# Optimization experiments

Hardware: AMD Instinct MI355X
Metric: run time of the kernel (lower is better)

## Reference

```python
import jax, jax.numpy as jnp
import numpy as np

NUM_HEADS = 12
NUM_LANDMARKS = 64
PINV_ITERS = 6


def moore_penrose_iter_pinv(x, iters=PINV_ITERS):
    # x: [..., m, m]
    abs_x = jnp.abs(x)
    col = abs_x.sum(axis=-1)
    row = abs_x.sum(axis=-2)
    z = jnp.swapaxes(x, -1, -2) / (jnp.max(col) * jnp.max(row))
    I = jnp.eye(x.shape[-1], dtype=x.dtype)
    for _ in range(iters):
        xz = x @ z
        z = 0.25 * z @ (13.0 * I - xz @ (15.0 * I - xz @ (7.0 * I - xz)))
    return z


def setup_inputs() -> dict:
    key = jax.random.key(0)
    k1, k2, k3, k4 = jax.random.split(key, 4)
    B, N, C = 2, 2048, 768
    x = jax.random.normal(k1, (B, N, C), dtype=jnp.float32)
    w_qkv = jax.random.normal(k2, (3 * C, C), dtype=jnp.float32) * 0.02
    w_proj = jax.random.normal(k3, (C, C), dtype=jnp.float32) * 0.02
    b_proj = jax.random.normal(k4, (C,), dtype=jnp.float32) * 0.02
    return {"x": x, "w_qkv": w_qkv, "w_proj": w_proj, "b_proj": b_proj}


def reference(x, w_qkv, w_proj, b_proj):
    B, N, C = x.shape
    H = NUM_HEADS
    m = NUM_LANDMARKS
    d = C // H
    scale = d ** -0.5
    original_N = N

    rem = N % m
    if rem > 0:  # pad at the FRONT of the sequence, as in the torch code
        x = jnp.pad(x, ((0, 0), (m - rem, 0), (0, 0)))
        N = x.shape[1]

    qkv = x @ w_qkv.T  # [B, N, 3C]
    q, k, v = jnp.split(qkv, 3, axis=-1)
    # [B, N, C] -> [B, H, N, d]
    to_heads = lambda t: t.reshape(B, N, H, d).transpose(0, 2, 1, 3)
    q, k, v = to_heads(q), to_heads(k), to_heads(v)
    q = q * scale

    l = N // m  # segment length per landmark (N is a multiple of m after padding)
    # '(n l) d -> n d' mean over l: landmarks [B, H, m, d]
    q_landmarks = q.reshape(B, H, m, l, d).mean(axis=3)
    k_landmarks = k.reshape(B, H, m, l, d).mean(axis=3)

    sim1 = jnp.einsum('bhnd,bhmd->bhnm', q, k_landmarks)          # [B,H,N,m]
    sim2 = jnp.einsum('bhid,bhjd->bhij', q_landmarks, k_landmarks)  # [B,H,m,m]
    sim3 = jnp.einsum('bhmd,bhnd->bhmn', q_landmarks, k)          # [B,H,m,N]

    attn1 = jax.nn.softmax(sim1, axis=-1)
    attn2 = jax.nn.softmax(sim2, axis=-1)
    attn3 = jax.nn.softmax(sim3, axis=-1)

    attn2_inv = moore_penrose_iter_pinv(attn2, PINV_ITERS)

    attn = (attn1 @ attn2_inv) @ attn3            # [B,H,N,N] full attention map
    out = attn1 @ (attn2_inv @ (attn3 @ v))       # [B,H,N,d]

    out = out.transpose(0, 2, 1, 3).reshape(B, N, C)
    out = out[:, -original_N:]
    out = out @ w_proj.T + b_proj
    return out, attn
```

## Files before the change

### kernel.cpp

```cpp
#include <hip/hip_runtime.h>
#include <math.h>

#define BQ 2
#define NQ 2048
#define CQ 768
#define HQ 12
#define DQ 64
#define MQ 64
#define LQ 32
#define C3 2304
#define BH 24
#define BN 4096

typedef short bf16x8 __attribute__((ext_vector_type(8)));
typedef float f32x4 __attribute__((ext_vector_type(4)));

__device__ inline void atomicMaxPosF(float* addr, float v) {
  atomicMax((int*)addr, __float_as_int(v));
}

__device__ inline void f2pair(float f, ushort& hi, ushort& lo) {
  union { float f; unsigned u; } a; a.f = f;
  hi = (ushort)(a.u >> 16);
  union { unsigned u; float f; } h; h.u = ((unsigned)hi) << 16;
  union { float f; unsigned u; } b; b.f = f - h.f;
  lo = (ushort)(b.u >> 16);
}

__device__ inline void stage_plane(const ushort* __restrict__ g, int ld,
                                   ushort* l, int t) {
#pragma unroll
  for (int i = 0; i < 4; ++i) {
    int flat = t + i * 256;
    int row = flat >> 3;
    int ch = (flat & 7) ^ (row & 7);
    __builtin_amdgcn_global_load_lds(
        (const __attribute__((address_space(1))) void*)(g + (size_t)row * ld + ch * 8),
        (__attribute__((address_space(3))) void*)(l + flat * 8), 16, 0, 0);
  }
}

__device__ inline bf16x8 rdfrag(const ushort* p, int row, int kb) {
  return *(const bf16x8*)((const char*)p + row * 128 + (kb ^ ((row & 7) << 4)));
}

__global__ __launch_bounds__(256) void gemm_bt3(
    const ushort* __restrict__ Ah, const ushort* __restrict__ Al,
    const ushort* __restrict__ Bh, const ushort* __restrict__ Bl,
    const float* __restrict__ bias, float* __restrict__ C,
    int Kdim, int lda, int ldb, int ldc, int qscale, int zH,
    long long sAb, long long sAh, long long sBb, long long sBh,
    long long sCb, long long sCh)
{
  __shared__ __align__(16) ushort lds[32768];
  ushort* LAh = lds;
  ushort* LAl = lds + 8192;
  ushort* LBh = lds + 16384;
  ushort* LBl = lds + 24576;
  const int t = threadIdx.x;
  const int z = blockIdx.z;
  const int b = z / zH, h = z % zH;
  const size_t aoff = (size_t)b * sAb + (size_t)h * sAh + (size_t)blockIdx.x * 128 * lda;
  const size_t boff = (size_t)b * sBb + (size_t)h * sBh + (size_t)blockIdx.y * 128 * ldb;
  const ushort* pAh = Ah + aoff;
  const ushort* pAl = Al + aoff;
  const ushort* pBh = Bh + boff;
  const ushort* pBl = Bl + boff;
  float* Cp = C + (size_t)b * sCb + (size_t)h * sCh;
  const int lane = t & 63, wv = t >> 6, wm = wv >> 1, wn = wv & 1;
  f32x4 zz = {0.f, 0.f, 0.f, 0.f};
  f32x4 acc[4][4] = {{zz, zz, zz, zz}, {zz, zz, zz, zz},
                     {zz, zz, zz, zz}, {zz, zz, zz, zz}};
  for (int k0 = 0; k0 < Kdim; k0 += 64) {
    stage_plane(pAh + k0, lda, LAh, t);
    stage_plane(pAl + k0, lda, LAl, t);
    stage_plane(pBh + k0, ldb, LBh, t);
    stage_plane(pBl + k0, ldb, LBl, t);
    __syncthreads();
#pragma unroll
    for (int kh = 0; kh < 2; ++kh) {
      const int kb = kh * 64 + ((lane >> 4) * 16);
      bf16x8 aH[4], aL[4], bHf[4], bLf[4];
#pragma unroll
      for (int i = 0; i < 4; ++i) {
        int ra = wm * 64 + i * 16 + (lane & 15);
        int rb = wn * 64 + i * 16 + (lane & 15);
        aH[i] = rdfrag(LAh, ra, kb);
        aL[i] = rdfrag(LAl, ra, kb);
        bHf[i] = rdfrag(LBh, rb, kb);
        bLf[i] = rdfrag(LBl, rb, kb);
      }
#pragma unroll
      for (int i = 0; i < 4; ++i)
#pragma unroll
        for (int j = 0; j < 4; ++j) {
          acc[i][j] = __builtin_amdgcn_mfma_f32_16x16x32_bf16(aH[i], bHf[j], acc[i][j], 0, 0, 0);
          acc[i][j] = __builtin_amdgcn_mfma_f32_16x16x32_bf16(aH[i], bLf[j], acc[i][j], 0, 0, 0);
          acc[i][j] = __builtin_amdgcn_mfma_f32_16x16x32_bf16(aL[i], bHf[j], acc[i][j], 0, 0, 0);
        }
    }
    __syncthreads();
  }
#pragma unroll
  for (int i = 0; i < 4; ++i)
#pragma unroll
    for (int j = 0; j < 4; ++j) {
      int row = blockIdx.x * 128 + wm * 64 + i * 16 + (lane >> 4) * 4;
      int col = blockIdx.y * 128 + wn * 64 + j * 16 + (lane & 15);
      float badd = bias ? bias[col] : 0.0f;
      float sc = (qscale && col < CQ) ? 0.125f : 1.0f;
#pragma unroll
      for (int r = 0; r < 4; ++r)
        Cp[(size_t)(row + r) * ldc + col] = acc[i][j][r] * sc + badd;
    }
}

__global__ void convert_planes(const float* __restrict__ src, ushort* __restrict__ hi,
                               ushort* __restrict__ lo, int n4)
{
  int i = blockIdx.x * 256 + threadIdx.x;
  if (i >= n4) return;
  float4 v = ((const float4*)src)[i];
  ushort4 H, L;
  f2pair(v.x, H.x, L.x); f2pair(v.y, H.y, L.y);
  f2pair(v.z, H.z, L.z); f2pair(v.w, H.w, L.w);
  ((ushort4*)hi)[i] = H;
  ((ushort4*)lo)[i] = L;
}

__device__ inline int swzb(int row, int kbyte) {
  return row * 128 + (kbyte ^ ((row & 7) << 4));
}

__device__ inline bf16x8 ldfrag(const ushort* plane, int row, int kbyte) {
  return *(const bf16x8*)((const char*)plane + swzb(row, kbyte));
}

__device__ inline void stage_nt(const float* __restrict__ src, int ld,
                                ushort* ph, ushort* pl, int t) {
#pragma unroll
  for (int rep = 0; rep < 4; ++rep) {
    int idx = t + rep * 256;
    int row = idx >> 4, f4 = idx & 15;
    float4 v = *(const float4*)(src + (size_t)row * ld + f4 * 4);
    ushort h0, h1, h2, h3, l0, l1, l2, l3;
    f2pair(v.x, h0, l0); f2pair(v.y, h1, l1);
    f2pair(v.z, h2, l2); f2pair(v.w, h3, l3);
    int byt = row * 128 + ((f4 * 8) ^ ((row & 7) << 4));
    *(ushort4*)((char*)ph + byt) = make_ushort4(h0, h1, h2, h3);
    *(ushort4*)((char*)pl + byt) = make_ushort4(l0, l1, l2, l3);
  }
}

__device__ inline void stage_nn(const float* __restrict__ src, int ld,
                                ushort* ph, ushort* pl, int t) {
#pragma unroll
  for (int rep = 0; rep < 4; ++rep) {
    int idx = t + rep * 256;
    int krow = idx >> 4, f4 = idx & 15;
    float4 v = *(const float4*)(src + (size_t)krow * ld + f4 * 4);
    float vv[4] = {v.x, v.y, v.z, v.w};
#pragma unroll
    for (int c = 0; c < 4; ++c) {
      int n = f4 * 4 + c;
      ushort hi, lo;
      f2pair(vv[c], hi, lo);
      int byt = n * 128 + ((krow * 2) ^ ((n & 7) << 4));
      *(ushort*)((char*)ph + byt) = hi;
      *(ushort*)((char*)pl + byt) = lo;
    }
  }
}

__device__ inline void tile_mma(const ushort* Ah, const ushort* Al,
                                const ushort* Bh, const ushort* Bl,
                                f32x4 acc[2][2], int lane, int wm, int wn) {
  bf16x8 aH[2][2], aL[2][2], bH[2][2], bL[2][2];
#pragma unroll
  for (int mi = 0; mi < 2; ++mi)
#pragma unroll
    for (int ki = 0; ki < 2; ++ki) {
      int kb = ki * 64 + ((lane >> 4) * 16);
      int ra = wm * 32 + mi * 16 + (lane & 15);
      int rb = wn * 32 + mi * 16 + (lane & 15);
      aH[mi][ki] = ldfrag(Ah, ra, kb);
      aL[mi][ki] = ldfrag(Al, ra, kb);
      bH[mi][ki] = ldfrag(Bh, rb, kb);
      bL[mi][ki] = ldfrag(Bl, rb, kb);
    }
#pragma unroll
  for (int mi = 0; mi < 2; ++mi)
#pragma unroll
    for (int ni = 0; ni < 2; ++ni)
#pragma unroll
      for (int ki = 0; ki < 2; ++ki) {
        acc[mi][ni] = __builtin_amdgcn_mfma_f32_16x16x32_bf16(
            aH[mi][ki], bH[ni][ki], acc[mi][ni], 0, 0, 0);
        acc[mi][ni] = __builtin_amdgcn_mfma_f32_16x16x32_bf16(
            aH[mi][ki], bL[ni][ki], acc[mi][ni], 0, 0, 0);
        acc[mi][ni] = __builtin_amdgcn_mfma_f32_16x16x32_bf16(
            aL[mi][ki], bH[ni][ki], acc[mi][ni], 0, 0, 0);
      }
}

__global__ __launch_bounds__(256) void gemm_heads_mfma(
    const float* __restrict__ A, const float* __restrict__ Bsrc,
    float* __restrict__ Cm,
    int kTilesPerSplit, int transB, int nBH,
    long long sAb, long long sAh, int lda,
    long long sBb, long long sBh, int ldb,
    long long sCb, long long sCh, int ldc, long long sCsplit,
    ushort* __restrict__ Hout, ushort* __restrict__ Lout)
{
  __shared__ __align__(16) ushort lds[16384];
  ushort* Ah = lds; ushort* Al = lds + 4096;
  ushort* Bh = lds + 8192; ushort* Bl = lds + 12288;
  const int t = threadIdx.x;
  const int z = blockIdx.z;
  const int split = z / nBH;
  const int bh = z % nBH;
  const int b = bh / HQ, h = bh % HQ;
  const float* Ap = A + (size_t)b * sAb + (size_t)h * sAh;
  const float* Bp = Bsrc + (size_t)b * sBb + (size_t)h * sBh;
  const int m0 = blockIdx.x * 64, n0 = blockIdx.y * 64;
  const int lane = t & 63, wv = t >> 6, wm = wv >> 1, wn = wv & 1;
  f32x4 zz = {0.f, 0.f, 0.f, 0.f};
  f32x4 acc[2][2] = {{zz, zz}, {zz, zz}};
  const int kbase = split * kTilesPerSplit * 64;
  for (int kt = 0; kt < kTilesPerSplit; ++kt) {
    int k0 = kbase + kt * 64;
    stage_nt(Ap + (size_t)m0 * lda + k0, lda, Ah, Al, t);
    if (transB)
      stage_nt(Bp + (size_t)n0 * ldb + k0, ldb, Bh, Bl, t);
    else
      stage_nn(Bp + (size_t)k0 * ldb + n0, ldb, Bh, Bl, t);
    __syncthreads();
    tile_mma(Ah, Al, Bh, Bl, acc, lane, wm, wn);
    __syncthreads();
  }
  if (Hout) {
    ushort* Hp = Hout + (size_t)b * sCb + (size_t)h * sCh + (size_t)split * sCsplit;
    ushort* Lp = Lout + (size_t)b * sCb + (size_t)h * sCh + (size_t)split * sCsplit;
#pragma unroll
    for (int mi = 0; mi < 2; ++mi)
#pragma unroll
      for (int ni = 0; ni < 2; ++ni) {
        int row = m0 + wm * 32 + mi * 16 + (lane >> 4) * 4;
        int col = n0 + wn * 32 + ni * 16 + (lane & 15);
#pragma unroll
        for (int r = 0; r < 4; ++r) {
          ushort hi, lo;
          f2pair(acc[mi][ni][r], hi, lo);
          Hp[(size_t)(row + r) * ldc + col] = hi;
          Lp[(size_t)(row + r) * ldc + col] = lo;
        }
      }
  } else {
    float* Cp = Cm + (size_t)b * sCb + (size_t)h * sCh + (size_t)split * sCsplit;
#pragma unroll
    for (int mi = 0; mi < 2; ++mi)
#pragma unroll
      for (int ni = 0; ni < 2; ++ni) {
        int row = m0 + wm * 32 + mi * 16 + (lane >> 4) * 4;
        int col = n0 + wn * 32 + ni * 16 + (lane & 15);
#pragma unroll
        for (int r = 0; r < 4; ++r)
          Cp[(size_t)(row + r) * ldc + col] = acc[mi][ni][r];
      }
  }
}

__global__ void landmarks_kernel(const float* __restrict__ qkv,
                                 float* __restrict__ ql, float* __restrict__ kl)
{
  int idx = blockIdx.x * 256 + threadIdx.x;
  int sel = idx / 98304;
  int r = idx % 98304;
  int bh = r / 4096;
  int b = bh / HQ, h = bh % HQ;
  int i = (r % 4096) / 64;
  int dd = r & 63;
  const float* base = qkv + (size_t)(b * NQ + i * LQ) * C3 + sel * CQ + h * 64 + dd;
  float s = 0.f;
#pragma unroll
  for (int j = 0; j < LQ; ++j) s += base[(size_t)j * C3];
  float* outp = sel ? kl : ql;
  outp[bh * 4096 + i * 64 + dd] = s * (1.0f / 32.0f);
}

__global__ __launch_bounds__(256) void attn2_prep(
    const float* __restrict__ ql, const float* __restrict__ kl,
    float* __restrict__ attn2, float* __restrict__ scal)
{
  __shared__ float Q[64][68], Kl[64][68], S[64][68];
  __shared__ float red[128];
  const int bh = blockIdx.x;
  const int t = threadIdx.x;
#pragma unroll
  for (int rep = 0; rep < 4; ++rep) {
    int idx = t + rep * 256;
    int row = idx >> 4, f4 = idx & 15;
    *(float4*)&Q[row][f4 * 4] = *(const float4*)(ql + (size_t)bh * 4096 + row * 64 + f4 * 4);
    *(float4*)&Kl[row][f4 * 4] = *(const float4*)(kl + (size_t)bh * 4096 + row * 64 + f4 * 4);
  }
  __syncthreads();
  {
    int i = t >> 2;
    int jb = (t & 3) * 16;
    for (int jj = 0; jj < 16; ++jj) {
      int j = jb + jj;
      float s2 = 0.f;
#pragma unroll
      for (int kk = 0; kk < 64; ++kk) s2 = fmaf(Q[i][kk], Kl[j][kk], s2);
      S[i][j] = s2;
    }
  }
  __syncthreads();
  if (t < 64) {
    float mx = -INFINITY;
    for (int j = 0; j < 64; ++j) mx = fmaxf(mx, S[t][j]);
    float sum = 0.f;
    for (int j = 0; j < 64; ++j) { float e = expf(S[t][j] - mx); S[t][j] = e; sum += e; }
    float inv = 1.0f / sum;
    float rs = 0.f;
    for (int j = 0; j < 64; ++j) { float v = S[t][j] * inv; S[t][j] = v; rs += v; }
    red[t] = rs;
  }
  __syncthreads();
  if (t < 64) {
    float cs = 0.f;
    for (int i = 0; i < 64; ++i) cs += S[i][t];
    red[64 + t] = cs;
  }
  __syncthreads();
  if (t == 0) {
    float m1 = red[0], m2 = red[64];
    for (int j = 1; j < 64; ++j) { m1 = fmaxf(m1, red[j]); m2 = fmaxf(m2, red[64 + j]); }
    atomicMaxPosF(scal + 0, m1);
    atomicMaxPosF(scal + 1, m2);
  }
  for (int idx = t; idx < 4096; idx += 256)
    attn2[(size_t)bh * 4096 + idx] = S[idx >> 6][idx & 63];
}

__device__ inline void mm64x(float (*D)[68], const float (*A)[68], const float (*B)[68],
                             int t, float scale)
{
  const int lane = t & 63, wv = t >> 6;
  float bcol[64];
#pragma unroll
  for (int kk = 0; kk < 64; ++kk) bcol[kk] = B[kk][lane];
#pragma unroll
  for (int rr = 0; rr < 4; ++rr) {
    int i = wv * 4 + rr;
    float acc2 = 0.f;
#pragma unroll
    for (int kk = 0; kk < 64; ++kk) acc2 = fmaf(A[i][kk], bcol[kk], acc2);
    D[i][lane] = acc2 * scale;
  }
}

__global__ __launch_bounds__(1024) void pinv_kernel(
    const float* __restrict__ attn2, const float* __restrict__ scal,
    float* __restrict__ zinv)
{
  __shared__ float X[64][68], Z[64][68], P[64][68], Q[64][68], R[64][68];
  const int bh = blockIdx.x;
  const int t = threadIdx.x;
  const float denom = scal[0] * scal[1];
#pragma unroll
  for (int rep = 0; rep < 4; ++rep) {
    int idx = t + rep * 1024;
    X[idx >> 6][idx & 63] = attn2[(size_t)bh * 4096 + idx];
  }
  __syncthreads();
#pragma unroll
  for (int rep = 0; rep < 4; ++rep) {
    int idx = t + rep * 1024;
    int i = idx >> 6, j = idx & 63;
    Z[j][i] = X[i][j] / denom;
  }
  for (int it = 0; it < 6; ++it) {
    __syncthreads();
    mm64x(P, X, Z, t, 1.0f);
    __syncthreads();
    for (int idx = t; idx < 4096; idx += 1024) {
      int i = idx >> 6, j = idx & 63;
      Q[i][j] = (i == j ? 7.0f : 0.0f) - P[i][j];
    }
    __syncthreads();
    mm64x(R, P, Q, t, 1.0f);
    __syncthreads();
    for (int idx = t; idx < 4096; idx += 1024) {
      int i = idx >> 6, j = idx & 63;
      Q[i][j] = (i == j ? 15.0f : 0.0f) - R[i][j];
    }
    __syncthreads();
    mm64x(R, P, Q, t, 1.0f);
    __syncthreads();
    for (int idx = t; idx < 4096; idx += 1024) {
      int i = idx >> 6, j = idx & 63;
      Q[i][j] = (i == j ? 13.0f : 0.0f) - R[i][j];
    }
    __syncthreads();
    mm64x(P, Z, Q, t, 0.25f);
    __syncthreads();
    for (int idx = t; idx < 4096; idx += 1024) {
      int i = idx >> 6, j = idx & 63;
      Z[i][j] = P[i][j];
    }
  }
  __syncthreads();
  for (int idx = t; idx < 4096; idx += 1024)
    zinv[(size_t)bh * 4096 + idx] = Z[idx >> 6][idx & 63];
}

__global__ __launch_bounds__(256) void attn1_kernel(
    const float* __restrict__ qkv, const float* __restrict__ kl,
    ushort* __restrict__ A1h, ushort* __restrict__ A1l)
{
  __shared__ float qs[64][68], klt[64][68];
  const int n0 = blockIdx.x * 64;
  const int bh = blockIdx.y;
  const int b = bh / HQ, h = bh % HQ;
  const int t = threadIdx.x;
#pragma unroll
  for (int rep = 0; rep < 4; ++rep) {
    int idx = t + rep * 256;
    int row = idx >> 4, f4 = idx & 15;
    *(float4*)&qs[row][f4 * 4] =
        *(const float4*)(qkv + (size_t)(b * NQ + n0 + row) * C3 + h * 64 + f4 * 4);
    float4 kv = *(const float4*)(kl + (size_t)bh * 4096 + row * 64 + f4 * 4);
    klt[f4 * 4 + 0][row] = kv.x; klt[f4 * 4 + 1][row] = kv.y;
    klt[f4 * 4 + 2][row] = kv.z; klt[f4 * 4 + 3][row] = kv.w;
  }
  __syncthreads();
  const int lane = t & 63, wv = t >> 6;
  float bcol[64];
#pragma unroll
  for (int kk = 0; kk < 64; ++kk) bcol[kk] = klt[kk][lane];
  for (int rr = 0; rr < 16; ++rr) {
    int i = wv * 16 + rr;
    float s = 0.f;
#pragma unroll
    for (int kk = 0; kk < 64; ++kk) s = fmaf(qs[i][kk], bcol[kk], s);
    float mx = s;
#pragma unroll
    for (int off = 32; off; off >>= 1) mx = fmaxf(mx, __shfl_xor(mx, off));
    float e = expf(s - mx);
    float sum = e;
#pragma unroll
    for (int off = 32; off; off >>= 1) sum += __shfl_xor(sum, off);
    float v = e / sum;
    ushort hi, lo;
    f2pair(v, hi, lo);
    size_t o = ((size_t)(b * NQ + n0 + i)) * CQ + h * 64 + lane;
    A1h[o] = hi;
    A1l[o] = lo;
  }
}

__global__ __launch_bounds__(256) void softmax2048(float* __restrict__ buf)
{
  __shared__ float red[8];
  const size_t base = (size_t)blockIdx.x * 2048;
  const int t = threadIdx.x;
  const int wv = t >> 6, lane = t & 63;
  float v[8];
  float mx = -INFINITY;
#pragma unroll
  for (int r = 0; r < 8; ++r) {
    v[r] = buf[base + t + r * 256];
    mx = fmaxf(mx, v[r]);
  }
#pragma unroll
  for (int off = 32; off; off >>= 1) mx = fmaxf(mx, __shfl_xor(mx, off));
  if (lane == 0) red[wv] = mx;
  __syncthreads();
  mx = fmaxf(fmaxf(red[0], red[1]), fmaxf(red[2], red[3]));
  float sum = 0.f;
#pragma unroll
  for (int r = 0; r < 8; ++r) { v[r] = expf(v[r] - mx); sum += v[r]; }
#pragma unroll
  for (int off = 32; off; off >>= 1) sum += __shfl_xor(sum, off);
  if (lane == 0) red[4 + wv] = sum;
  __syncthreads();
  float total = (red[4] + red[5]) + (red[6] + red[7]);
  float inv = 1.0f / total;
#pragma unroll
  for (int r = 0; r < 8; ++r) buf[base + t + r * 256] = v[r] * inv;
}

__global__ void reduce8_kernel(const float* __restrict__ part, float* __restrict__ outp)
{
  int idx = blockIdx.x * 256 + threadIdx.x;
  float s = 0.f;
#pragma unroll
  for (int r = 0; r < 8; ++r) s += part[(size_t)r * 98304 + idx];
  outp[idx] = s;
}

__global__ __launch_bounds__(256) void transpose_T(
    const float* __restrict__ TBm, ushort* __restrict__ TTh, ushort* __restrict__ TTl)
{
  __shared__ float S[64][65];
  const int bh = blockIdx.y;
  const int n0 = blockIdx.x * 64;
  const int t = threadIdx.x;
  const float* src = TBm + (size_t)bh * 131072 + n0;
#pragma unroll
  for (int i = 0; i < 16; ++i) {
    int idx = t + i * 256;
    int m = idx >> 6, nn = idx & 63;
    S[m][nn] = src[(size_t)m * 2048 + nn];
  }
  __syncthreads();
  ushort* dh = TTh + (size_t)bh * 131072 + (size_t)n0 * 64;
  ushort* dl = TTl + (size_t)bh * 131072 + (size_t)n0 * 64;
#pragma unroll
  for (int i = 0; i < 16; ++i) {
    int idx = t + i * 256;
    int nn = idx >> 6, m = idx & 63;
    ushort hi, lo;
    f2pair(S[m][nn], hi, lo);
    dh[(size_t)nn * 64 + m] = hi;
    dl[(size_t)nn * 64 + m] = lo;
  }
}

__global__ void init_scal(float* s)
{
  if (threadIdx.x < 2) s[threadIdx.x] = 0.0f;
}

extern "C" void kernel_launch(void* const* d_in, const int* in_sizes, int n_in,
                              void* d_out, int out_size, void* d_ws, size_t ws_size,
                              hipStream_t stream)
{
  const float* x = (const float*)d_in[0];
  const float* w_qkv = (const float*)d_in[1];
  const float* w_proj = (const float*)d_in[2];
  const float* b_proj = (const float*)d_in[3];
  float* out = (float*)d_out;
  float* R = out + (size_t)BQ * NQ * CQ;

  float* QKV = R;
  float* AT3 = R + 9437184;
  float* TBm = R + 12582912;
  float* W3P = R + 15728640;
  float* W3V = R + 16515072;
  float* UU  = R + 16613376;
  ushort* xp_h = (ushort*)(R + 16711680);
  ushort* xp_l = xp_h + 3145728;
  ushort* wq_h = xp_l + 3145728;
  ushort* wq_l = wq_h + 1769472;
  ushort* gt_h = wq_l + 1769472;
  ushort* gt_l = gt_h + 1179648;

  float* ws = (float*)d_ws;
  float* QL = ws;
  float* KL = QL + 98304;
  float* A2 = KL + 98304;
  float* ZI = A2 + 98304;
  float* SC = ZI + 98304;
  ushort* a1_h = (ushort*)(SC + 32);
  ushort* a1_l = a1_h + 3145728;
  ushort* tt_h = a1_l + 3145728;
  ushort* tt_l = tt_h + 3145728;

  init_scal<<<1, 64, 0, stream>>>(SC);

  convert_planes<<<3072, 256, 0, stream>>>(x, xp_h, xp_l, 786432);
  convert_planes<<<1728, 256, 0, stream>>>(w_qkv, wq_h, wq_l, 442368);

  gemm_bt3<<<dim3(32, 18, 1), 256, 0, stream>>>(
      xp_h, xp_l, wq_h, wq_l, nullptr, QKV,
      CQ, CQ, CQ, C3, 1, 1, 0, 0, 0, 0, 0, 0);

  landmarks_kernel<<<768, 256, 0, stream>>>(QKV, QL, KL);
  attn2_prep<<<24, 256, 0, stream>>>(QL, KL, A2, SC);
  pinv_kernel<<<24, 1024, 0, stream>>>(A2, SC, ZI);
  attn1_kernel<<<dim3(32, 24), 256, 0, stream>>>(QKV, KL, a1_h, a1_l);

  gemm_heads_mfma<<<dim3(1, 32, 24), 256, 0, stream>>>(
      QL, QKV + CQ, AT3, 1, 1, 24,
      (long long)HQ * 4096, 4096, 64,
      (long long)NQ * C3, 64, C3,
      (long long)HQ * 131072, 131072, 2048, 0, nullptr, nullptr);
  softmax2048<<<1536, 256, 0, stream>>>(AT3);

  gemm_heads_mfma<<<dim3(1, 1, 192), 256, 0, stream>>>(
      AT3, QKV + 2 * CQ, W3P, 4, 0, 24,
      (long long)HQ * 131072, 131072, 2048,
      (long long)NQ * C3, 64, C3,
      (long long)HQ * 4096, 4096, 64, (long long)24 * 4096, nullptr, nullptr);
  reduce8_kernel<<<384, 256, 0, stream>>>(W3P, W3V);

  gemm_heads_mfma<<<dim3(1, 1, 24), 256, 0, stream>>>(
      ZI, W3V, UU, 1, 0, 24,
      (long long)HQ * 4096, 4096, 64,
      (long long)HQ * 4096, 4096, 64,
      (long long)HQ * 4096, 4096, 64, 0, nullptr, nullptr);

  gemm_heads_mfma<<<dim3(12, 1, 24), 256, 0, stream>>>(
      w_proj, UU, nullptr, 1, 1, 24,
      0, 64, CQ,
      (long long)HQ * 4096, 4096, 64,
      (long long)CQ * CQ, 64, CQ, 0, gt_h, gt_l);

  gemm_heads_mfma<<<dim3(1, 32, 24), 256, 0, stream>>>(
      ZI, AT3, TBm, 1, 0, 24,
      (long long)HQ * 4096, 4096, 64,
      (long long)HQ * 131072, 131072, 2048,
      (long long)HQ * 131072, 131072, 2048, 0, nullptr, nullptr);
  transpose_T<<<dim3(32, 24), 256, 0, stream>>>(TBm, tt_h, tt_l);

  gemm_bt3<<<dim3(16, 6, 2), 256, 0, stream>>>(
      a1_h, a1_l, gt_h, gt_l, b_proj, out,
      CQ, CQ, CQ, CQ, 0, 1,
      (long long)NQ * CQ, 0, (long long)CQ * CQ, 0, (long long)NQ * CQ, 0);

  gemm_bt3<<<dim3(16, 16, 24), 256, 0, stream>>>(
      a1_h, a1_l, tt_h, tt_l, nullptr, R,
      64, CQ, 64, 2048, 0, HQ,
      (long long)NQ * CQ, 64,
      (long long)HQ * 131072, 131072,
      (long long)HQ * 4194304LL, 4194304);
}
```

Baseline: 381.5 us.

## Fuse sim3 softmax chain and fold row normalization into pinv matrix

Replaces the sim3 GEMM, the 2048-wide softmax, the split-K attn3@v GEMM with its reduce, the Z@W3 GEMM, the Z@attn3 GEMM and the transpose with three kernels. The first kernel computes exp(q_l·k) per 64-token chunk and writes per-chunk row sums, E@v partials and a transposed bf16 split of E. The second kernel sums the partials and folds the softmax denominators into Z by scaling its columns. The third computes the T chunks directly in the transposed split-bf16 layout. This removes the round trips of the fp32 [m, N] attn3 buffer and several launches, but it drops the max subtraction in the softmax and uses fast __expf, which risks overflow or precision loss for large logits.

```diff
diff --git a/kernel.cpp b/kernel.cpp
--- a/kernel.cpp
+++ b/kernel.cpp
@@ -460,71 +460,196 @@
   }
 }
 
-__global__ __launch_bounds__(256) void softmax2048(float* __restrict__ buf)
-{
-  __shared__ float red[8];
-  const size_t base = (size_t)blockIdx.x * 2048;
+__global__ __launch_bounds__(256) void sim3_fused(
+    const float* __restrict__ ql, const float* __restrict__ qkv,
+    ushort* __restrict__ eth, ushort* __restrict__ etl,
+    float* __restrict__ rspart, float* __restrict__ evp)
+{
+  __shared__ __align__(16) ushort lds[32768];
+  __shared__ float rsq[2][64];
+  const int chunk = blockIdx.x, bh = blockIdx.y;
+  const int b = bh / HQ, h = bh % HQ;
+  const int n0 = chunk * 64;
   const int t = threadIdx.x;
-  const int wv = t >> 6, lane = t & 63;
-  float v[8];
-  float mx = -INFINITY;
-#pragma unroll
-  for (int r = 0; r < 8; ++r) {
-    v[r] = buf[base + t + r * 256];
-    mx = fmaxf(mx, v[r]);
-  }
-#pragma unroll
-  for (int off = 32; off; off >>= 1) mx = fmaxf(mx, __shfl_xor(mx, off));
-  if (lane == 0) red[wv] = mx;
-  __syncthreads();
-  mx = fmaxf(fmaxf(red[0], red[1]), fmaxf(red[2], red[3]));
-  float sum = 0.f;
-#pragma unroll
-  for (int r = 0; r < 8; ++r) { v[r] = expf(v[r] - mx); sum += v[r]; }
-#pragma unroll
-  for (int off = 32; off; off >>= 1) sum += __shfl_xor(sum, off);
-  if (lane == 0) red[4 + wv] = sum;
-  __syncthreads();
-  float total = (red[4] + red[5]) + (red[6] + red[7]);
-  float inv = 1.0f / total;
-#pragma unroll
-  for (int r = 0; r < 8; ++r) buf[base + t + r * 256] = v[r] * inv;
-}
-
-__global__ void reduce8_kernel(const float* __restrict__ part, float* __restrict__ outp)
-{
-  int idx = blockIdx.x * 256 + threadIdx.x;
-  float s = 0.f;
-#pragma unroll
-  for (int r = 0; r < 8; ++r) s += part[(size_t)r * 98304 + idx];
-  outp[idx] = s;
-}
-
-__global__ __launch_bounds__(256) void transpose_T(
-    const float* __restrict__ TBm, ushort* __restrict__ TTh, ushort* __restrict__ TTl)
-{
-  __shared__ float S[64][65];
-  const int bh = blockIdx.y;
-  const int n0 = blockIdx.x * 64;
+  const int lane = t & 63, wv = t >> 6, wm = wv >> 1, wn = wv & 1;
+  ushort* Aqh = lds;         ushort* Aql = lds + 4096;
+  ushort* Bkh = lds + 8192;  ushort* Bkl = lds + 12288;
+  ushort* EH  = lds + 16384; ushort* EL  = lds + 20480;
+  ushort* ETH = lds + 24576; ushort* ETL = lds + 28672;
+  ushort* vTh = lds;         ushort* vTl = lds + 4096;
+
+  stage_nt(ql + (size_t)bh * 4096, 64, Aqh, Aql, t);
+  stage_nt(qkv + (size_t)(b * NQ + n0) * C3 + CQ + h * 64, C3, Bkh, Bkl, t);
+  __syncthreads();
+  f32x4 zz = {0.f, 0.f, 0.f, 0.f};
+  f32x4 acc[2][2] = {{zz, zz}, {zz, zz}};
+  tile_mma(Aqh, Aql, Bkh, Bkl, acc, lane, wm, wn);
+  float e[2][2][4];
+#pragma unroll
+  for (int mi = 0; mi < 2; ++mi)
+#pragma unroll
+    for (int ni = 0; ni < 2; ++ni)
+#pragma unroll
+      for (int r = 0; r < 4; ++r) {
+        float ev = __expf(acc[mi][ni][r]);
+        e[mi][ni][r] = ev;
+        int m = wm * 32 + mi * 16 + ((lane >> 4) << 2) + r;
+        int n = wn * 32 + ni * 16 + (lane & 15);
+        ushort hi, lo;
+        f2pair(ev, hi, lo);
+        *(ushort*)((char*)EH + swzb(m, n * 2)) = hi;
+        *(ushort*)((char*)EL + swzb(m, n * 2)) = lo;
+        *(ushort*)((char*)ETH + swzb(n, m * 2)) = hi;
+        *(ushort*)((char*)ETL + swzb(n, m * 2)) = lo;
+      }
+#pragma unroll
+  for (int mi = 0; mi < 2; ++mi)
+#pragma unroll
+    for (int r = 0; r < 4; ++r) {
+      float s = e[mi][0][r] + e[mi][1][r];
+      s += __shfl_xor(s, 1); s += __shfl_xor(s, 2);
+      s += __shfl_xor(s, 4); s += __shfl_xor(s, 8);
+      if ((lane & 15) == 0)
+        rsq[wn][wm * 32 + mi * 16 + ((lane >> 4) << 2) + r] = s;
+    }
+  __syncthreads();
+  stage_nn(qkv + (size_t)(b * NQ + n0) * C3 + 2 * CQ + h * 64, C3, vTh, vTl, t);
+  if (t < 64)
+    rspart[(size_t)(bh * 32 + chunk) * 64 + t] = rsq[0][t] + rsq[1][t];
+  {
+    ushort* gh = eth + (size_t)(bh * 32 + chunk) * 4096;
+    ushort* gl = etl + (size_t)(bh * 32 + chunk) * 4096;
+#pragma unroll
+    for (int r2 = 0; r2 < 2; ++r2) {
+      int c8 = t + r2 * 256;
+      *(bf16x8*)(gh + c8 * 8) = *(const bf16x8*)(ETH + c8 * 8);
+      *(bf16x8*)(gl + c8 * 8) = *(const bf16x8*)(ETL + c8 * 8);
+    }
+  }
+  __syncthreads();
+  f32x4 acc2[2][2] = {{zz, zz}, {zz, zz}};
+  tile_mma(EH, EL, vTh, vTl, acc2, lane, wm, wn);
+  float* evpp = evp + (size_t)(bh * 32 + chunk) * 4096;
+#pragma unroll
+  for (int mi = 0; mi < 2; ++mi)
+#pragma unroll
+    for (int ni = 0; ni < 2; ++ni) {
+      int m = wm * 32 + mi * 16 + ((lane >> 4) << 2);
+      int d = wn * 32 + ni * 16 + (lane & 15);
+#pragma unroll
+      for (int r = 0; r < 4; ++r)
+        evpp[(m + r) * 64 + d] = acc2[mi][ni][r];
+    }
+}
+
+__global__ __launch_bounds__(256) void pinv_apply(
+    const float* __restrict__ rspart, const float* __restrict__ evp,
+    const float* __restrict__ zinv, float* __restrict__ uu,
+    ushort* __restrict__ zph, ushort* __restrict__ zpl)
+{
+  __shared__ __align__(16) ushort lds[16384];
+  __shared__ float rs[64];
+  ushort* EvTh = lds;        ushort* EvTl = lds + 4096;
+  ushort* ZAh  = lds + 8192; ushort* ZAl  = lds + 12288;
+  const int bh = blockIdx.x;
   const int t = threadIdx.x;
-  const float* src = TBm + (size_t)bh * 131072 + n0;
-#pragma unroll
-  for (int i = 0; i < 16; ++i) {
-    int idx = t + i * 256;
-    int m = idx >> 6, nn = idx & 63;
-    S[m][nn] = src[(size_t)m * 2048 + nn];
-  }
-  __syncthreads();
-  ushort* dh = TTh + (size_t)bh * 131072 + (size_t)n0 * 64;
-  ushort* dl = TTl + (size_t)bh * 131072 + (size_t)n0 * 64;
-#pragma unroll
-  for (int i = 0; i < 16; ++i) {
-    int idx = t + i * 256;
-    int nn = idx >> 6, m = idx & 63;
+  const int lane = t & 63, wv = t >> 6, wm = wv >> 1, wn = wv & 1;
+  if (t < 64) {
+    float s = 0.f;
+#pragma unroll
+    for (int c = 0; c < 32; ++c) s += rspart[(size_t)(bh * 32 + c) * 64 + t];
+    rs[t] = s;
+  }
+#pragma unroll
+  for (int rep = 0; rep < 16; ++rep) {
+    int idx = t + rep * 256;
+    int m = idx >> 6, d = idx & 63;
+    float s = 0.f;
+    for (int c = 0; c < 32; ++c) s += evp[(size_t)(bh * 32 + c) * 4096 + idx];
     ushort hi, lo;
-    f2pair(S[m][nn], hi, lo);
-    dh[(size_t)nn * 64 + m] = hi;
-    dl[(size_t)nn * 64 + m] = lo;
+    f2pair(s, hi, lo);
+    *(ushort*)((char*)EvTh + swzb(d, m * 2)) = hi;
+    *(ushort*)((char*)EvTl + swzb(d, m * 2)) = lo;
+  }
+  __syncthreads();
+#pragma unroll
+  for (int rep = 0; rep < 16; ++rep) {
+    int idx = t + rep * 256;
+    int i = idx >> 6, m = idx & 63;
+    float v = zinv[(size_t)bh * 4096 + idx] / rs[m];
+    ushort hi, lo;
+    f2pair(v, hi, lo);
+    *(ushort*)((char*)ZAh + swzb(i, m * 2)) = hi;
+    *(ushort*)((char*)ZAl + swzb(i, m * 2)) = lo;
+  }
+  __syncthreads();
+  f32x4 zz = {0.f, 0.f, 0.f, 0.f};
+  f32x4 acc[2][2] = {{zz, zz}, {zz, zz}};
+  tile_mma(ZAh, ZAl, EvTh, EvTl, acc, lane, wm, wn);
+#pragma unroll
+  for (int mi = 0; mi < 2; ++mi)
+#pragma unroll
+    for (int ni = 0; ni < 2; ++ni) {
+      int i = wm * 32 + mi * 16 + ((lane >> 4) << 2);
+      int d = wn * 32 + ni * 16 + (lane & 15);
+#pragma unroll
+      for (int r = 0; r < 4; ++r)
+        uu[(size_t)bh * 4096 + (i + r) * 64 + d] = acc[mi][ni][r];
+    }
+#pragma unroll
+  for (int r2 = 0; r2 < 2; ++r2) {
+    int c8 = t + r2 * 256;
+    *(bf16x8*)(zph + (size_t)bh * 4096 + c8 * 8) = *(const bf16x8*)(ZAh + c8 * 8);
+    *(bf16x8*)(zpl + (size_t)bh * 4096 + c8 * 8) = *(const bf16x8*)(ZAl + c8 * 8);
+  }
+}
+
+__global__ __launch_bounds__(256) void t_chunk_kernel(
+    const ushort* __restrict__ zph, const ushort* __restrict__ zpl,
+    const ushort* __restrict__ eth, const ushort* __restrict__ etl,
+    ushort* __restrict__ tth, ushort* __restrict__ ttl)
+{
+  __shared__ __align__(16) ushort lds[16384];
+  __shared__ float Tt[64][65];
+  ushort* ZAh = lds;        ushort* ZAl = lds + 4096;
+  ushort* EBh = lds + 8192; ushort* EBl = lds + 12288;
+  const int chunk = blockIdx.x, bh = blockIdx.y;
+  const int t = threadIdx.x;
+  const int lane = t & 63, wv = t >> 6, wm = wv >> 1, wn = wv & 1;
+  const ushort* geh = eth + (size_t)(bh * 32 + chunk) * 4096;
+  const ushort* gel = etl + (size_t)(bh * 32 + chunk) * 4096;
+#pragma unroll
+  for (int r2 = 0; r2 < 2; ++r2) {
+    int c8 = t + r2 * 256;
+    *(bf16x8*)(ZAh + c8 * 8) = *(const bf16x8*)(zph + (size_t)bh * 4096 + c8 * 8);
+    *(bf16x8*)(ZAl + c8 * 8) = *(const bf16x8*)(zpl + (size_t)bh * 4096 + c8 * 8);
+    *(bf16x8*)(EBh + c8 * 8) = *(const bf16x8*)(geh + c8 * 8);
+    *(bf16x8*)(EBl + c8 * 8) = *(const bf16x8*)(gel + c8 * 8);
+  }
+  __syncthreads();
+  f32x4 zz = {0.f, 0.f, 0.f, 0.f};
+  f32x4 acc[2][2] = {{zz, zz}, {zz, zz}};
+  tile_mma(ZAh, ZAl, EBh, EBl, acc, lane, wm, wn);
+#pragma unroll
+  for (int mi = 0; mi < 2; ++mi)
+#pragma unroll
+    for (int ni = 0; ni < 2; ++ni) {
+      int i = wm * 32 + mi * 16 + ((lane >> 4) << 2);
+      int n = wn * 32 + ni * 16 + (lane & 15);
+#pragma unroll
+      for (int r = 0; r < 4; ++r)
+        Tt[i + r][n] = acc[mi][ni][r];
+    }
+  __syncthreads();
+  const size_t base = ((size_t)bh * 2048 + chunk * 64) * 64;
+#pragma unroll
+  for (int rep = 0; rep < 16; ++rep) {
+    int idx = t + rep * 256;
+    int n = idx >> 6, i = idx & 63;
+    ushort hi, lo;
+    f2pair(Tt[i][n], hi, lo);
+    tth[base + n * 64 + i] = hi;
+    ttl[base + n * 64 + i] = lo;
   }
 }
 
@@ -545,12 +670,14 @@
   float* R = out + (size_t)BQ * NQ * CQ;
 
   float* QKV = R;
-  float* AT3 = R + 9437184;
-  float* TBm = R + 12582912;
-  float* W3P = R + 15728640;
-  float* W3V = R + 16515072;
-  float* UU  = R + 16613376;
-  ushort* xp_h = (ushort*)(R + 16711680);
+  float* EVP = R + 9437184;
+  float* UU  = R + 12582912;
+  float* RSP = R + 12681216;
+  ushort* et_h = (ushort*)(R + 12730368);
+  ushort* et_l = et_h + 3145728;
+  ushort* zp_h = et_l + 3145728;
+  ushort* zp_l = zp_h + 98304;
+  ushort* xp_h = zp_l + 98304;
   ushort* xp_l = xp_h + 3145728;
   ushort* wq_h = xp_l + 3145728;
   ushort* wq_l = wq_h + 1769472;
@@ -582,38 +709,14 @@
   pinv_kernel<<<24, 1024, 0, stream>>>(A2, SC, ZI);
   attn1_kernel<<<dim3(32, 24), 256, 0, stream>>>(QKV, KL, a1_h, a1_l);
 
-  gemm_heads_mfma<<<dim3(1, 32, 24), 256, 0, stream>>>(
-      QL, QKV + CQ, AT3, 1, 1, 24,
-      (long long)HQ * 4096, 4096, 64,
-      (long long)NQ * C3, 64, C3,
-      (long long)HQ * 131072, 131072, 2048, 0, nullptr, nullptr);
-  softmax2048<<<1536, 256, 0, stream>>>(AT3);
-
-  gemm_heads_mfma<<<dim3(1, 1, 192), 256, 0, stream>>>(
-      AT3, QKV + 2 * CQ, W3P, 4, 0, 24,
-      (long long)HQ * 131072, 131072, 2048,
-      (long long)NQ * C3, 64, C3,
-      (long long)HQ * 4096, 4096, 64, (long long)24 * 4096, nullptr, nullptr);
-  reduce8_kernel<<<384, 256, 0, stream>>>(W3P, W3V);
-
-  gemm_heads_mfma<<<dim3(1, 1, 24), 256, 0, stream>>>(
-      ZI, W3V, UU, 1, 0, 24,
-      (long long)HQ * 4096, 4096, 64,
-      (long long)HQ * 4096, 4096, 64,
-      (long long)HQ * 4096, 4096, 64, 0, nullptr, nullptr);
-
+  sim3_fused<<<dim3(32, 24), 256, 0, stream>>>(QL, QKV, et_h, et_l, RSP, EVP);
+  pinv_apply<<<24, 256, 0, stream>>>(RSP, EVP, ZI, UU, zp_h, zp_l);
   gemm_heads_mfma<<<dim3(12, 1, 24), 256, 0, stream>>>(
       w_proj, UU, nullptr, 1, 1, 24,
       0, 64, CQ,
       (long long)HQ * 4096, 4096, 64,
       (long long)CQ * CQ, 64, CQ, 0, gt_h, gt_l);
-
-  gemm_heads_mfma<<<dim3(1, 32, 24), 256, 0, stream>>>(
-      ZI, AT3, TBm, 1, 0, 24,
-      (long long)HQ * 4096, 4096, 64,
-      (long long)HQ * 131072, 131072, 2048,
-      (long long)HQ * 131072, 131072, 2048, 0, nullptr, nullptr);
-  transpose_T<<<dim3(32, 24), 256, 0, stream>>>(TBm, tt_h, tt_l);
+  t_chunk_kernel<<<dim3(32, 24), 256, 0, stream>>>(zp_h, zp_l, et_h, et_l, tt_h, tt_l);
 
   gemm_bt3<<<dim3(16, 6, 2), 256, 0, stream>>>(
       a1_h, a1_l, gt_h, gt_l, b_proj, out,
```

After: 465.0 us. 1.22x slower.

## Fuse sim3 GEMM with exp and fold softmax normalization into pinv output

Applied to the files above, without the earlier changes.

Replaces the sim3 GEMM and the separate row-softmax pass with a single kernel that runs the MFMA tile, writes exp(scores) unnormalized, and emits partial row sums. A small reduction kernel finishes the row sums. Each column of the pinv result is then divided by the matching row sum, so the 1/rowsum scaling moves into the 64x64 inverse instead of the 24x64x2048 map. This removes a full read-modify-write pass over the attn3 buffer and one launch. The trade-off is that the max subtraction is dropped, so exp of large scores could overflow.

```diff
diff --git a/kernel.cpp b/kernel.cpp
--- a/kernel.cpp
+++ b/kernel.cpp
@@ -270,6 +270,65 @@
   }
 }
 
+__global__ __launch_bounds__(256) void sim3_exp(
+    const float* __restrict__ ql, const float* __restrict__ qkv,
+    float* __restrict__ E, float* __restrict__ rspart)
+{
+  __shared__ __align__(16) ushort lds[16384];
+  __shared__ float rsq[2][64];
+  ushort* Ah = lds; ushort* Al = lds + 4096;
+  ushort* Bh = lds + 8192; ushort* Bl = lds + 12288;
+  const int chunk = blockIdx.x, bh = blockIdx.y;
+  const int b = bh / HQ, h = bh % HQ;
+  const int t = threadIdx.x;
+  const int lane = t & 63, wv = t >> 6, wm = wv >> 1, wn = wv & 1;
+  stage_nt(ql + (size_t)bh * 4096, 64, Ah, Al, t);
+  stage_nt(qkv + (size_t)(b * NQ + chunk * 64) * C3 + CQ + h * 64, C3, Bh, Bl, t);
+  __syncthreads();
+  f32x4 zz = {0.f, 0.f, 0.f, 0.f};
+  f32x4 acc[2][2] = {{zz, zz}, {zz, zz}};
+  tile_mma(Ah, Al, Bh, Bl, acc, lane, wm, wn);
+  float* Cp = E + (size_t)bh * 131072 + chunk * 64;
+  float e[2][2][4];
+#pragma unroll
+  for (int mi = 0; mi < 2; ++mi)
+#pragma unroll
+    for (int ni = 0; ni < 2; ++ni) {
+      int row = wm * 32 + mi * 16 + (lane >> 4) * 4;
+      int col = wn * 32 + ni * 16 + (lane & 15);
+#pragma unroll
+      for (int r = 0; r < 4; ++r) {
+        float ev = __expf(acc[mi][ni][r]);
+        e[mi][ni][r] = ev;
+        Cp[(size_t)(row + r) * 2048 + col] = ev;
+      }
+    }
+#pragma unroll
+  for (int mi = 0; mi < 2; ++mi)
+#pragma unroll
+    for (int r = 0; r < 4; ++r) {
+      float s = e[mi][0][r] + e[mi][1][r];
+      s += __shfl_xor(s, 1); s += __shfl_xor(s, 2);
+      s += __shfl_xor(s, 4); s += __shfl_xor(s, 8);
+      if ((lane & 15) == 0)
+        rsq[wn][wm * 32 + mi * 16 + ((lane >> 4) << 2) + r] = s;
+    }
+  __syncthreads();
+  if (t < 64)
+    rspart[(size_t)(bh * 32 + chunk) * 64 + t] = rsq[0][t] + rsq[1][t];
+}
+
+__global__ void rs_final(const float* __restrict__ rspart, float* __restrict__ rsf)
+{
+  int g = blockIdx.x * 256 + threadIdx.x;
+  if (g >= 1536) return;
+  int bh = g >> 6, j = g & 63;
+  float s = 0.f;
+#pragma unroll
+  for (int c = 0; c < 32; ++c) s += rspart[(size_t)(bh * 32 + c) * 64 + j];
+  rsf[g] = s;
+}
+
 __global__ void landmarks_kernel(const float* __restrict__ qkv,
                                  float* __restrict__ ql, float* __restrict__ kl)
 {
@@ -362,7 +421,7 @@
 
 __global__ __launch_bounds__(1024) void pinv_kernel(
     const float* __restrict__ attn2, const float* __restrict__ scal,
-    float* __restrict__ zinv)
+    const float* __restrict__ rsf, float* __restrict__ zinv)
 {
   __shared__ float X[64][68], Z[64][68], P[64][68], Q[64][68], R[64][68];
   const int bh = blockIdx.x;
@@ -412,7 +471,7 @@
   }
   __syncthreads();
   for (int idx = t; idx < 4096; idx += 1024)
-    zinv[(size_t)bh * 4096 + idx] = Z[idx >> 6][idx & 63];
+    zinv[(size_t)bh * 4096 + idx] = Z[idx >> 6][idx & 63] / rsf[bh * 64 + (idx & 63)];
 }
 
 __global__ __launch_bounds__(256) void attn1_kernel(
@@ -460,37 +519,6 @@
   }
 }
 
-__global__ __launch_bounds__(256) void softmax2048(float* __restrict__ buf)
-{
-  __shared__ float red[8];
-  const size_t base = (size_t)blockIdx.x * 2048;
-  const int t = threadIdx.x;
-  const int wv = t >> 6, lane = t & 63;
-  float v[8];
-  float mx = -INFINITY;
-#pragma unroll
-  for (int r = 0; r < 8; ++r) {
-    v[r] = buf[base + t + r * 256];
-    mx = fmaxf(mx, v[r]);
-  }
-#pragma unroll
-  for (int off = 32; off; off >>= 1) mx = fmaxf(mx, __shfl_xor(mx, off));
-  if (lane == 0) red[wv] = mx;
-  __syncthreads();
-  mx = fmaxf(fmaxf(red[0], red[1]), fmaxf(red[2], red[3]));
-  float sum = 0.f;
-#pragma unroll
-  for (int r = 0; r < 8; ++r) { v[r] = expf(v[r] - mx); sum += v[r]; }
-#pragma unroll
-  for (int off = 32; off; off >>= 1) sum += __shfl_xor(sum, off);
-  if (lane == 0) red[4 + wv] = sum;
-  __syncthreads();
-  float total = (red[4] + red[5]) + (red[6] + red[7]);
-  float inv = 1.0f / total;
-#pragma unroll
-  for (int r = 0; r < 8; ++r) buf[base + t + r * 256] = v[r] * inv;
-}
-
 __global__ void reduce8_kernel(const float* __restrict__ part, float* __restrict__ outp)
 {
   int idx = blockIdx.x * 256 + threadIdx.x;
@@ -550,7 +578,9 @@
   float* W3P = R + 15728640;
   float* W3V = R + 16515072;
   float* UU  = R + 16613376;
-  ushort* xp_h = (ushort*)(R + 16711680);
+  float* RSP = R + 16711680;
+  float* RSF = R + 16760832;
+  ushort* xp_h = (ushort*)(R + 16762368);
   ushort* xp_l = xp_h + 3145728;
   ushort* wq_h = xp_l + 3145728;
   ushort* wq_l = wq_h + 1769472;
@@ -579,15 +609,13 @@
 
   landmarks_kernel<<<768, 256, 0, stream>>>(QKV, QL, KL);
   attn2_prep<<<24, 256, 0, stream>>>(QL, KL, A2, SC);
-  pinv_kernel<<<24, 1024, 0, stream>>>(A2, SC, ZI);
+
+  sim3_exp<<<dim3(32, 24), 256, 0, stream>>>(QL, QKV, AT3, RSP);
+  rs_final<<<6, 256, 0, stream>>>(RSP, RSF);
+
+  pinv_kernel<<<24, 1024, 0, stream>>>(A2, SC, RSF, ZI);
+
   attn1_kernel<<<dim3(32, 24), 256, 0, stream>>>(QKV, KL, a1_h, a1_l);
-
-  gemm_heads_mfma<<<dim3(1, 32, 24), 256, 0, stream>>>(
-      QL, QKV + CQ, AT3, 1, 1, 24,
-      (long long)HQ * 4096, 4096, 64,
-      (long long)NQ * C3, 64, C3,
-      (long long)HQ * 131072, 131072, 2048, 0, nullptr, nullptr);
-  softmax2048<<<1536, 256, 0, stream>>>(AT3);
 
   gemm_heads_mfma<<<dim3(1, 1, 192), 256, 0, stream>>>(
       AT3, QKV + 2 * CQ, W3P, 4, 0, 24,
```

After: 380.3 us (median of 2 runs). No clear change (-0.3%).
